# Optimization experiments

Hardware: AMD Instinct MI355X
Metric: run time of the kernel (lower is better)

The kernel has to match this reference:

```python
import jax, jax.numpy as jnp
import numpy as np

WS = 16      # window_size
FW = 1       # focal_window -> 3x3 grid of focal windows
FF = 2       # focal_factor (avg-pool for non-center windows)
NH = 8       # num_heads

_OFFSETS = [(di, dj) for di in range(-FW, FW + 1) for dj in range(-FW, FW + 1)]
# tokens contributed by each focal window (center keeps full res, neighbors pooled)
_COUNTS = np.array([WS * WS if (di == 0 and dj == 0) else (WS // FF) ** 2 for di, dj in _OFFSETS])
# center window gets zero bias, peripheral windows get -position_bias (intent of add_focal_bias)
_MULTS = np.array([0.0 if (di == 0 and dj == 0) else -1.0 for di, dj in _OFFSETS], dtype=np.float32)


def _gather_focal(x):
    """x: (B,H,W,C) -> (B*nW, kv_len, C) focal key/value tokens per window."""
    B, H, W, C = x.shape
    nH, nWg = H // WS, W // WS
    xp = jnp.pad(x, ((0, 0), (WS, WS), (WS, WS), (0, 0)), mode='reflect')
    # padded window grid: (B, nH+2, nWg+2, WS, WS, C)
    g = xp.reshape(B, nH + 2, WS, nWg + 2, WS, C).transpose(0, 1, 3, 2, 4, 5)
    parts = []
    for di, dj in _OFFSETS:
        w = g[:, 1 + di:1 + di + nH, 1 + dj:1 + dj + nWg]  # (B,nH,nWg,WS,WS,C)
        if di == 0 and dj == 0:
            t = w.reshape(B, nH, nWg, WS * WS, C)
        else:
            p = WS // FF  # avg_pool2d(kernel=stride=FF)
            t = w.reshape(B, nH, nWg, p, FF, p, FF, C).mean(axis=(4, 6)).reshape(B, nH, nWg, p * p, C)
        parts.append(t)
    kv = jnp.concatenate(parts, axis=3)  # (B,nH,nWg,kv_len,C)
    return kv.reshape(B * nH * nWg, -1, C)


def _bias_tokens(position_bias):
    # (NH, 9) -> (NH, kv_len): per-focal-window bias broadcast over its tokens
    scaled = position_bias * jnp.asarray(_MULTS)[None, :]
    return jnp.repeat(scaled, _COUNTS, axis=1)


def reference(x, Wq, bq, Wk, bk, Wv, bv, Wo, bo, position_bias):
    B, H, W, C = x.shape
    hd = C // NH
    scale = hd ** -0.5
    nH, nWg = H // WS, W // WS
    # window partition: (B*nW, WS*WS, C)
    xw = x.reshape(B, nH, WS, nWg, WS, C).transpose(0, 1, 3, 2, 4, 5).reshape(-1, WS * WS, C)
    kv = _gather_focal(x)  # (B*nW, kv_len, C)
    q = (xw @ Wq + bq).reshape(-1, WS * WS, NH, hd).transpose(0, 2, 1, 3)
    k = (kv @ Wk + bk).reshape(kv.shape[0], -1, NH, hd).transpose(0, 2, 1, 3)
    v = (kv @ Wv + bv).reshape(kv.shape[0], -1, NH, hd).transpose(0, 2, 1, 3)
    attn = jnp.einsum('whqd,whkd->whqk', q, k) * scale
    attn = attn + _bias_tokens(position_bias)[None, :, None, :]
    attn = jax.nn.softmax(attn, axis=-1)
    out = jnp.einsum('whqk,whkd->whqd', attn, v).transpose(0, 2, 1, 3).reshape(-1, WS * WS, C)
    out = out @ Wo + bo
    # window reverse
    out = out.reshape(B, nH, nWg, WS, WS, C).transpose(0, 1, 3, 2, 4, 5).reshape(B, H, W, C)
    return out


def setup_inputs() -> dict:
    key = jax.random.key(0)
    ks = jax.random.split(key, 10)
    D = 384
    w = lambda k: jax.random.normal(k, (D, D), dtype=jnp.float32) * 0.02
    b = lambda k: jax.random.normal(k, (D,), dtype=jnp.float32) * 0.02
    return {
        'x': jax.random.normal(ks[0], (2, 128, 128, D), dtype=jnp.float32),
        'Wq': w(ks[1]), 'bq': b(ks[2]),
        'Wk': w(ks[3]), 'bk': b(ks[4]),
        'Wv': w(ks[5]), 'bv': b(ks[6]),
        'Wo': w(ks[7]), 'bo': b(ks[8]),
        'position_bias': jax.random.normal(ks[9], (NH, 9), dtype=jnp.float32) * 0.02,
    }
```

## Files before the change

### kernel.cpp

```cpp
#include <hip/hip_runtime.h>
#include <hip/hip_bf16.h>

#define NTOK 32768
#define LOG2E 1.4426950408889634f

typedef __attribute__((ext_vector_type(8))) short bf16x8;
typedef __attribute__((ext_vector_type(4))) float f32x4;

__device__ __forceinline__ float bf2f(unsigned short u) {
  return __uint_as_float(((unsigned int)u) << 16);
}
__device__ __forceinline__ unsigned short f2bf(float f) {
  union { __hip_bfloat16 h; unsigned short u; } cv;
  cv.h = __float2bfloat16(f);
  return cv.u;
}
__device__ __forceinline__ unsigned cvt_pk_bf16(float lo, float hi) {
  unsigned r;
  asm("v_cvt_pk_bf16_f32 %0, %1, %2" : "=v"(r) : "v"(lo), "v"(hi));
  return r;
}
__device__ __forceinline__ float fast_exp2(float x) {
#if __has_builtin(__builtin_amdgcn_exp2f)
  return __builtin_amdgcn_exp2f(x);
#else
  return exp2f(x);
#endif
}

__device__ __forceinline__ void gload16(const void* g, void* l) {
  __builtin_amdgcn_global_load_lds(
      (const __attribute__((address_space(1))) unsigned int*)(unsigned long long)g,
      (__attribute__((address_space(3))) unsigned int*)(unsigned long long)l, 16, 0, 0);
}

__global__ __launch_bounds__(256) void convert_x(const float* __restrict__ x,
                                                 unsigned short* __restrict__ xb) {
  const int i = (blockIdx.x * 256 + threadIdx.x) * 8;
  float4 a = *(const float4*)(x + i);
  float4 b = *(const float4*)(x + i + 4);
  *(ushort4*)(xb + i)     = make_ushort4(f2bf(a.x), f2bf(a.y), f2bf(a.z), f2bf(a.w));
  *(ushort4*)(xb + i + 4) = make_ushort4(f2bf(b.x), f2bf(b.y), f2bf(b.z), f2bf(b.w));
}

__global__ __launch_bounds__(256) void transpose_w(const float* __restrict__ Wq,
                                                   const float* __restrict__ Wk,
                                                   const float* __restrict__ Wv,
                                                   const float* __restrict__ Wo,
                                                   unsigned short* __restrict__ Wt) {
  __shared__ float tile[32][33];
  const int wsel = blockIdx.z;
  const float* W = (wsel == 0) ? Wq : (wsel == 1) ? Wk : (wsel == 2) ? Wv : Wo;
  unsigned short* out = Wt + (size_t)wsel * 147456;
  const int k0 = blockIdx.x * 32, n0 = blockIdx.y * 32;
  const int r = threadIdx.x >> 3, c4 = (threadIdx.x & 7) * 4;
  float4 v = *(const float4*)&W[(size_t)(k0 + r) * 384 + n0 + c4];
  tile[r][c4 + 0] = v.x; tile[r][c4 + 1] = v.y; tile[r][c4 + 2] = v.z; tile[r][c4 + 3] = v.w;
  __syncthreads();
  ushort4 o = make_ushort4(f2bf(tile[c4 + 0][r]), f2bf(tile[c4 + 1][r]),
                           f2bf(tile[c4 + 2][r]), f2bf(tile[c4 + 3][r]));
  *(ushort4*)&out[(size_t)(n0 + r) * 384 + k0 + c4] = o;
}

__global__ __launch_bounds__(192) void pool_kernel(const unsigned short* __restrict__ xb,
                                                   unsigned short* __restrict__ P) {
  const int unit = blockIdx.x * 192 + threadIdx.x;
  const int cell = unit / 48;
  const int c8 = (unit - cell * 48) * 8;
  const int b = cell / 6400;
  const int rem = cell - b * 6400;
  const int p0 = rem / 80, p1 = rem - p0 * 80;
  const int i0 = 2 * p0 - 16, i1 = i0 + 1;
  const int j0 = 2 * p1 - 16, j1 = j0 + 1;
  const int r0 = i0 < 0 ? -i0 : (i0 > 127 ? 254 - i0 : i0);
  const int r1 = i1 < 0 ? -i1 : (i1 > 127 ? 254 - i1 : i1);
  const int c0 = j0 < 0 ? -j0 : (j0 > 127 ? 254 - j0 : j0);
  const int c1 = j1 < 0 ? -j1 : (j1 > 127 ? 254 - j1 : j1);
  uint4 u00 = *(const uint4*)(xb + ((size_t)((b * 128 + r0) * 128 + c0)) * 384 + c8);
  uint4 u01 = *(const uint4*)(xb + ((size_t)((b * 128 + r0) * 128 + c1)) * 384 + c8);
  uint4 u10 = *(const uint4*)(xb + ((size_t)((b * 128 + r1) * 128 + c0)) * 384 + c8);
  uint4 u11 = *(const uint4*)(xb + ((size_t)((b * 128 + r1) * 128 + c1)) * 384 + c8);
  const unsigned short* a0 = (const unsigned short*)&u00;
  const unsigned short* a1 = (const unsigned short*)&u01;
  const unsigned short* a2 = (const unsigned short*)&u10;
  const unsigned short* a3 = (const unsigned short*)&u11;
  unsigned short o[8];
  #pragma unroll
  for (int j = 0; j < 8; ++j)
    o[j] = f2bf(0.25f * (bf2f(a0[j]) + bf2f(a1[j]) + bf2f(a2[j]) + bf2f(a3[j])));
  uint4 ov;
  unsigned short* op = (unsigned short*)&ov;
  #pragma unroll
  for (int j = 0; j < 8; ++j) op[j] = o[j];
  *(uint4*)(P + (size_t)cell * 384 + c8) = ov;
}

__global__ __launch_bounds__(256) void mfma_proj_fused(
    const unsigned short* __restrict__ xb, const unsigned short* __restrict__ P,
    const unsigned short* __restrict__ Wt,
    const float* __restrict__ bq, const float* __restrict__ bk, const float* __restrict__ bv,
    unsigned short* __restrict__ Qb, unsigned short* __restrict__ Kcat,
    unsigned short* __restrict__ Vcat) {
  const int bid = blockIdx.x;
  const unsigned short* X;
  int wsel, colblk, yy; size_t off;
  if (bid < 2304) {
    const int xx = bid % 9; yy = bid / 9;
    X = xb; wsel = xx / 3; colblk = xx % 3; off = 0;
  } else {
    const int r = bid - 2304; const int xx = r % 6; yy = r / 6;
    X = P; wsel = 1 + xx / 3; colblk = xx % 3; off = (size_t)NTOK * 384;
  }
  const float* bias = (wsel == 0) ? bq : (wsel == 1) ? bk : bv;
  unsigned short* Y = ((wsel == 0) ? Qb : (wsel == 1) ? Kcat : Vcat) + off;
  const unsigned short* Wm = Wt + (size_t)wsel * 147456;
  const int n0 = colblk * 128;
  const int m0 = yy * 128;

  __shared__ __attribute__((aligned(16))) unsigned short As[2][128 * 32];
  __shared__ __attribute__((aligned(16))) unsigned short Bs[2][128 * 32];
  const int t = threadIdx.x;
  const int w = t >> 6, l = t & 63, l15 = l & 15, g = l >> 4;
  const int wm = w >> 1, wn = w & 1;
  const int srow = (w * 2) * 16 + (l >> 2), srow2 = (w * 2 + 1) * 16 + (l >> 2);
  const int skc = (l & 3) * 8;

  f32x4 acc[4][4];
  #pragma unroll
  for (int i = 0; i < 4; ++i)
    #pragma unroll
    for (int j = 0; j < 4; ++j) acc[i][j] = {0.f, 0.f, 0.f, 0.f};

  {
    gload16(X  + (size_t)(m0 + srow)  * 384 + skc, &As[0][(w * 2)     * 512]);
    gload16(X  + (size_t)(m0 + srow2) * 384 + skc, &As[0][(w * 2 + 1) * 512]);
    gload16(Wm + (size_t)(n0 + srow)  * 384 + skc, &Bs[0][(w * 2)     * 512]);
    gload16(Wm + (size_t)(n0 + srow2) * 384 + skc, &Bs[0][(w * 2 + 1) * 512]);
  }
  asm volatile("s_waitcnt vmcnt(0)" ::: "memory");
  __builtin_amdgcn_s_barrier();
  __builtin_amdgcn_sched_barrier(0);

  int cur = 0;
  for (int kt = 0; kt < 12; ++kt) {
    if (kt < 11) {
      const int k0 = (kt + 1) * 32;
      gload16(X  + (size_t)(m0 + srow)  * 384 + k0 + skc, &As[cur ^ 1][(w * 2)     * 512]);
      gload16(X  + (size_t)(m0 + srow2) * 384 + k0 + skc, &As[cur ^ 1][(w * 2 + 1) * 512]);
      gload16(Wm + (size_t)(n0 + srow)  * 384 + k0 + skc, &Bs[cur ^ 1][(w * 2)     * 512]);
      gload16(Wm + (size_t)(n0 + srow2) * 384 + k0 + skc, &Bs[cur ^ 1][(w * 2 + 1) * 512]);
    }
    bf16x8 af[4], bfr[4];
    #pragma unroll
    for (int mi = 0; mi < 4; ++mi)
      af[mi] = *(const bf16x8*)(&As[cur][(wm * 64 + mi * 16 + l15) * 32 + g * 8]);
    #pragma unroll
    for (int nj = 0; nj < 4; ++nj)
      bfr[nj] = *(const bf16x8*)(&Bs[cur][(wn * 64 + nj * 16 + l15) * 32 + g * 8]);
    #pragma unroll
    for (int mi = 0; mi < 4; ++mi)
      #pragma unroll
      for (int nj = 0; nj < 4; ++nj)
        acc[mi][nj] = __builtin_amdgcn_mfma_f32_16x16x32_bf16(af[mi], bfr[nj], acc[mi][nj], 0, 0, 0);
    if (kt < 11) {
      asm volatile("s_waitcnt vmcnt(0)" ::: "memory");
      __builtin_amdgcn_s_barrier();
      __builtin_amdgcn_sched_barrier(0);
      cur ^= 1;
    }
  }

  float bv4[4];
  #pragma unroll
  for (int nj = 0; nj < 4; ++nj) bv4[nj] = bias[n0 + wn * 64 + nj * 16 + l15];
  #pragma unroll
  for (int mi = 0; mi < 4; ++mi)
    #pragma unroll
    for (int nj = 0; nj < 4; ++nj)
      #pragma unroll
      for (int r = 0; r < 4; ++r) {
        const size_t row = m0 + wm * 64 + mi * 16 + g * 4 + r;
        const size_t col = n0 + wn * 64 + nj * 16 + l15;
        Y[row * 384 + col] = f2bf(acc[mi][nj][r] + bv4[nj]);
      }
}

__global__ __launch_bounds__(256) void mfma_proj_out(const unsigned short* __restrict__ X,
                                                     const unsigned short* __restrict__ Wm,
                                                     const float* __restrict__ bias,
                                                     float* __restrict__ Y) {
  const int n0 = blockIdx.x * 128, m0 = blockIdx.y * 128;
  __shared__ __attribute__((aligned(16))) unsigned short As[2][128 * 32];
  __shared__ __attribute__((aligned(16))) unsigned short Bs[2][128 * 32];
  const int t = threadIdx.x;
  const int w = t >> 6, l = t & 63, l15 = l & 15, g = l >> 4;
  const int wm = w >> 1, wn = w & 1;
  const int srow = (w * 2) * 16 + (l >> 2), srow2 = (w * 2 + 1) * 16 + (l >> 2);
  const int skc = (l & 3) * 8;

  f32x4 acc[4][4];
  #pragma unroll
  for (int i = 0; i < 4; ++i)
    #pragma unroll
    for (int j = 0; j < 4; ++j) acc[i][j] = {0.f, 0.f, 0.f, 0.f};

  {
    gload16(X  + (size_t)(m0 + srow)  * 384 + skc, &As[0][(w * 2)     * 512]);
    gload16(X  + (size_t)(m0 + srow2) * 384 + skc, &As[0][(w * 2 + 1) * 512]);
    gload16(Wm + (size_t)(n0 + srow)  * 384 + skc, &Bs[0][(w * 2)     * 512]);
    gload16(Wm + (size_t)(n0 + srow2) * 384 + skc, &Bs[0][(w * 2 + 1) * 512]);
  }
  asm volatile("s_waitcnt vmcnt(0)" ::: "memory");
  __builtin_amdgcn_s_barrier();
  __builtin_amdgcn_sched_barrier(0);

  int cur = 0;
  for (int kt = 0; kt < 12; ++kt) {
    if (kt < 11) {
      const int k0 = (kt + 1) * 32;
      gload16(X  + (size_t)(m0 + srow)  * 384 + k0 + skc, &As[cur ^ 1][(w * 2)     * 512]);
      gload16(X  + (size_t)(m0 + srow2) * 384 + k0 + skc, &As[cur ^ 1][(w * 2 + 1) * 512]);
      gload16(Wm + (size_t)(n0 + srow)  * 384 + k0 + skc, &Bs[cur ^ 1][(w * 2)     * 512]);
      gload16(Wm + (size_t)(n0 + srow2) * 384 + k0 + skc, &Bs[cur ^ 1][(w * 2 + 1) * 512]);
    }
    bf16x8 af[4], bfr[4];
    #pragma unroll
    for (int mi = 0; mi < 4; ++mi)
      af[mi] = *(const bf16x8*)(&As[cur][(wm * 64 + mi * 16 + l15) * 32 + g * 8]);
    #pragma unroll
    for (int nj = 0; nj < 4; ++nj)
      bfr[nj] = *(const bf16x8*)(&Bs[cur][(wn * 64 + nj * 16 + l15) * 32 + g * 8]);
    #pragma unroll
    for (int mi = 0; mi < 4; ++mi)
      #pragma unroll
      for (int nj = 0; nj < 4; ++nj)
        acc[mi][nj] = __builtin_amdgcn_mfma_f32_16x16x32_bf16(af[mi], bfr[nj], acc[mi][nj], 0, 0, 0);
    if (kt < 11) {
      asm volatile("s_waitcnt vmcnt(0)" ::: "memory");
      __builtin_amdgcn_s_barrier();
      __builtin_amdgcn_sched_barrier(0);
      cur ^= 1;
    }
  }

  float bv4[4];
  #pragma unroll
  for (int nj = 0; nj < 4; ++nj) bv4[nj] = bias[n0 + wn * 64 + nj * 16 + l15];
  #pragma unroll
  for (int mi = 0; mi < 4; ++mi)
    #pragma unroll
    for (int nj = 0; nj < 4; ++nj)
      #pragma unroll
      for (int r = 0; r < 4; ++r) {
        const size_t row = m0 + wm * 64 + mi * 16 + g * 4 + r;
        const size_t col = n0 + wn * 64 + nj * 16 + l15;
        Y[row * 384 + col] = acc[mi][nj][r] + bv4[nj];
      }
}

__global__ __launch_bounds__(256) void attn_mfma(const unsigned short* __restrict__ Qg,
                                                 const unsigned short* __restrict__ Kc,
                                                 const unsigned short* __restrict__ Vc,
                                                 const float* __restrict__ pb,
                                                 unsigned short* __restrict__ AttO) {
  __shared__ unsigned short kvb[768];
  __shared__ float tb2s[12];
  __shared__ __attribute__((aligned(16))) unsigned short Ks[2][3072];
  __shared__ __attribute__((aligned(16))) unsigned short Vt[2][64 * 68];

  const int t = threadIdx.x;
  const int head = blockIdx.x >> 7, win = blockIdx.x & 127;
  const int b = win >> 6, wrem = win & 63, wi = wrem >> 3, wj = wrem & 7;
  const int w = t >> 6, l = t & 63, l15 = l & 15, g = l >> 4;
  const int hb = head * 48;

  for (int j = t; j < 768; j += 256) {
    int o, within;
    if (j < 256)      { o = j >> 6;               within = j & 63; }
    else if (j < 512) { o = 4;                    within = j - 256; }
    else              { o = 5 + ((j - 512) >> 6); within = j & 63; }
    int tok;
    if (o == 4) {
      int r = within >> 4, c = within & 15;
      tok = (b * 128 + wi * 16 + r) * 128 + wj * 16 + c;
    } else {
      int di = o / 3 - 1, dj = o - (o / 3) * 3 - 1;
      int t0 = within >> 3, t1 = within & 7;
      int p0 = 8 * (1 + di + wi) + t0, p1 = 8 * (1 + dj + wj) + t1;
      tok = NTOK + (b * 80 + p0) * 80 + p1;
    }
    kvb[j] = (unsigned short)tok;
  }
  if (t < 12) {
    int o = (t < 4) ? t : ((t < 8) ? 4 : t - 3);
    tb2s[t] = (o == 4) ? 0.0f : (-pb[head * 9 + o] * LOG2E);
  }
  for (int idx = t; idx < 2 * 16 * 68; idx += 256) {
    const int bu = idx / 1088, rem = idx - bu * 1088;
    const int rr = rem / 68, cc = rem - rr * 68;
    Vt[bu][(48 + rr) * 68 + cc] = (rr == 0) ? 0x3F80 : 0;
  }

  const float SCALE2 = 0.14433756729740643f * LOG2E;
  const bf16x8 z8 = {0, 0, 0, 0, 0, 0, 0, 0};

  bf16x8 qf[4][2];
  #pragma unroll
  for (int nf = 0; nf < 4; ++nf) {
    const int tok = ((b * 128 + wi * 16 + w * 4 + nf) * 128 + wj * 16 + l15);
    const unsigned short* qp = Qg + (size_t)tok * 384 + hb;
    qf[nf][0] = *(const bf16x8*)(qp + g * 8);
    qf[nf][1] = (g < 2) ? *(const bf16x8*)(qp + 32 + g * 8) : z8;
  }

  f32x4 Oacc[4][4];
  #pragma unroll
  for (int mo = 0; mo < 4; ++mo)
    #pragma unroll
    for (int nf = 0; nf < 4; ++nf) Oacc[mo][nf] = {0.f, 0.f, 0.f, 0.f};

  __syncthreads();

  uint4 va0, va1;
  {
    const int kvb0 = (int)kvb[l] * 384 + hb;
    gload16(Kc + kvb0 + w * 8, &Ks[0][w * 512]);
    if (w < 2) gload16(Kc + kvb0 + (4 + w) * 8, &Ks[0][(4 + w) * 512]);
    va0 = *(const uint4*)(Vc + kvb0 + w * 8);
    va1 = (w < 2) ? *(const uint4*)(Vc + kvb0 + (4 + w) * 8) : make_uint4(0, 0, 0, 0);
  }

  for (int T = 0; T < 12; ++T) {
    const int buf = T & 1;
    asm volatile("s_waitcnt vmcnt(0)" ::: "memory");
    {
      const unsigned short* u0 = (const unsigned short*)&va0;
      #pragma unroll
      for (int s = 0; s < 8; ++s) Vt[buf][(w * 8 + s) * 68 + l] = u0[s];
      if (w < 2) {
        const unsigned short* u1 = (const unsigned short*)&va1;
        #pragma unroll
        for (int s = 0; s < 8; ++s) Vt[buf][((4 + w) * 8 + s) * 68 + l] = u1[s];
      }
    }
    __syncthreads();
    if (T < 11) {
      const int kvb2 = (int)kvb[(T + 1) * 64 + l] * 384 + hb;
      gload16(Kc + kvb2 + w * 8, &Ks[buf ^ 1][w * 512]);
      if (w < 2) gload16(Kc + kvb2 + (4 + w) * 8, &Ks[buf ^ 1][(4 + w) * 512]);
      va0 = *(const uint4*)(Vc + kvb2 + w * 8);
      if (w < 2) va1 = *(const uint4*)(Vc + kvb2 + (4 + w) * 8);
    }

    const float tb = tb2s[T];
    #pragma unroll
    for (int h = 0; h < 2; ++h) {
      bf16x8 ka[2][2];
      #pragma unroll
      for (int mi = 0; mi < 2; ++mi) {
        const int krow = h * 32 + mi * 16 + l15;
        ka[mi][0] = *(const bf16x8*)&Ks[buf][g * 512 + krow * 8];
        ka[mi][1] = *(const bf16x8*)&Ks[buf][(4 + (g & 1)) * 512 + krow * 8];
      }
      f32x4 sf[2][4];
      #pragma unroll
      for (int mi = 0; mi < 2; ++mi)
        #pragma unroll
        for (int nf = 0; nf < 4; ++nf) sf[mi][nf] = {0.f, 0.f, 0.f, 0.f};
      __builtin_amdgcn_s_setprio(1);
      #pragma unroll
      for (int mi = 0; mi < 2; ++mi)
        #pragma unroll
        for (int nf = 0; nf < 4; ++nf) {
          sf[mi][nf] = __builtin_amdgcn_mfma_f32_16x16x32_bf16(ka[mi][0], qf[nf][0], sf[mi][nf], 0, 0, 0);
          sf[mi][nf] = __builtin_amdgcn_mfma_f32_16x16x32_bf16(ka[mi][1], qf[nf][1], sf[mi][nf], 0, 0, 0);
        }
      __builtin_amdgcn_s_setprio(0);

      bf16x8 pbf[4];
      #pragma unroll
      for (int nf = 0; nf < 4; ++nf) {
        float p[8];
        #pragma unroll
        for (int r = 0; r < 4; ++r) {
          p[r]     = fast_exp2(fmaf(sf[0][nf][r], SCALE2, tb));
          p[4 + r] = fast_exp2(fmaf(sf[1][nf][r], SCALE2, tb));
        }
        unsigned a0 = cvt_pk_bf16(p[0], p[1]);
        unsigned a1 = cvt_pk_bf16(p[2], p[3]);
        unsigned b0 = cvt_pk_bf16(p[4], p[5]);
        unsigned b1 = cvt_pk_bf16(p[6], p[7]);
        asm("v_permlane32_swap_b32 %0, %1" : "+v"(a0), "+v"(b0));
        asm("v_permlane32_swap_b32 %0, %1" : "+v"(a1), "+v"(b1));
        asm("v_permlane16_swap_b32 %0, %1" : "+v"(a0), "+v"(b0));
        asm("v_permlane16_swap_b32 %0, %1" : "+v"(a1), "+v"(b1));
        union { bf16x8 v; unsigned u[4]; } cv;
        cv.u[0] = a0; cv.u[1] = a1; cv.u[2] = b0; cv.u[3] = b1;
        pbf[nf] = cv.v;
      }

      #pragma unroll
      for (int mo = 0; mo < 4; ++mo) {
        const unsigned short* vp = &Vt[buf][(mo * 16 + l15) * 68 + h * 32 + g * 8];
        union { bf16x8 v; ushort4 u[2]; } cv;
        cv.u[0] = *(const ushort4*)vp;
        cv.u[1] = *(const ushort4*)(vp + 4);
        bf16x8 va = cv.v;
        __builtin_amdgcn_s_setprio(1);
        #pragma unroll
        for (int nf = 0; nf < 4; ++nf)
          Oacc[mo][nf] = __builtin_amdgcn_mfma_f32_16x16x32_bf16(va, pbf[nf], Oacc[mo][nf], 0, 0, 0);
        __builtin_amdgcn_s_setprio(0);
      }
    }
  }

  #pragma unroll
  for (int nf = 0; nf < 4; ++nf) {
    const float denom = __shfl(Oacc[3][nf][0], l15, 64);
    const float inv = 1.0f / denom;
    const int tok = ((b * 128 + wi * 16 + w * 4 + nf) * 128 + wj * 16 + l15);
    unsigned short* op = AttO + (size_t)tok * 384 + hb;
    #pragma unroll
    for (int mo = 0; mo < 3; ++mo) {
      uint2 u;
      u.x = cvt_pk_bf16(Oacc[mo][nf][0] * inv, Oacc[mo][nf][1] * inv);
      u.y = cvt_pk_bf16(Oacc[mo][nf][2] * inv, Oacc[mo][nf][3] * inv);
      *(uint2*)(op + mo * 16 + g * 4) = u;
    }
  }
}

extern "C" void kernel_launch(void* const* d_in, const int* in_sizes, int n_in,
                              void* d_out, int out_size, void* d_ws, size_t ws_size,
                              hipStream_t stream) {
  const float* x  = (const float*)d_in[0];
  const float* Wq = (const float*)d_in[1];
  const float* bq = (const float*)d_in[2];
  const float* Wk = (const float*)d_in[3];
  const float* bk = (const float*)d_in[4];
  const float* Wv = (const float*)d_in[5];
  const float* bv = (const float*)d_in[6];
  const float* Wo = (const float*)d_in[7];
  const float* bo = (const float*)d_in[8];
  const float* pb = (const float*)d_in[9];

  char* ws = (char*)d_ws;
  unsigned short* Wt   = (unsigned short*)(ws);
  unsigned short* P    = (unsigned short*)(ws + 1179648ull);
  unsigned short* Kcat = (unsigned short*)(ws + 11010048ull);
  unsigned short* Vcat = (unsigned short*)(ws + 46006272ull);
  unsigned short* xb   = (unsigned short*)(ws + 81002496ull);
  unsigned short* AttO = xb;
  unsigned short* Qb   = (unsigned short*)d_out;

  convert_x<<<6144, 256, 0, stream>>>(x, xb);
  pool_kernel<<<3200, 192, 0, stream>>>(xb, P);
  transpose_w<<<dim3(12, 12, 4), 256, 0, stream>>>(Wq, Wk, Wv, Wo, Wt);
  mfma_proj_fused<<<2904, 256, 0, stream>>>(xb, P, Wt, bq, bk, bv, Qb, Kcat, Vcat);
  attn_mfma<<<1024, 256, 0, stream>>>(Qb, Kcat, Vcat, pb, AttO);
  mfma_proj_out<<<dim3(3, 256), 256, 0, stream>>>(AttO, Wt + 3 * 147456, bo, (float*)d_out);
}
```

Baseline: 189.1 us.

## Triple-buffer GEMM K-tiles with two-deep prefetch and remap attention block order

Both projection GEMM kernels move from double to triple buffering in shared memory. Two K-tiles are prefetched ahead, and each iteration waits with vmcnt(4) rather than vmcnt(0), so one tile's loads stay in flight while the current tile is computed. The attention kernel also remaps block index to (head, window) so that 8 consecutive blocks share a head and cover neighbouring windows, aiming for better L2 reuse of overlapping K/V. The extra buffer raises LDS use per block, which may lower occupancy.

```diff
diff --git a/kernel.cpp b/kernel.cpp
--- a/kernel.cpp
+++ b/kernel.cpp
@@ -117,8 +117,8 @@
   const int n0 = colblk * 128;
   const int m0 = yy * 128;
 
-  __shared__ __attribute__((aligned(16))) unsigned short As[2][128 * 32];
-  __shared__ __attribute__((aligned(16))) unsigned short Bs[2][128 * 32];
+  __shared__ __attribute__((aligned(16))) unsigned short As[3][128 * 32];
+  __shared__ __attribute__((aligned(16))) unsigned short Bs[3][128 * 32];
   const int t = threadIdx.x;
   const int w = t >> 6, l = t & 63, l15 = l & 15, g = l >> 4;
   const int wm = w >> 1, wn = w & 1;
@@ -131,25 +131,29 @@
     #pragma unroll
     for (int j = 0; j < 4; ++j) acc[i][j] = {0.f, 0.f, 0.f, 0.f};
 
-  {
-    gload16(X  + (size_t)(m0 + srow)  * 384 + skc, &As[0][(w * 2)     * 512]);
-    gload16(X  + (size_t)(m0 + srow2) * 384 + skc, &As[0][(w * 2 + 1) * 512]);
-    gload16(Wm + (size_t)(n0 + srow)  * 384 + skc, &Bs[0][(w * 2)     * 512]);
-    gload16(Wm + (size_t)(n0 + srow2) * 384 + skc, &Bs[0][(w * 2 + 1) * 512]);
-  }
-  asm volatile("s_waitcnt vmcnt(0)" ::: "memory");
-  __builtin_amdgcn_s_barrier();
-  __builtin_amdgcn_sched_barrier(0);
-
-  int cur = 0;
+  #pragma unroll
+  for (int pt = 0; pt < 2; ++pt) {
+    const int k0 = pt * 32;
+    gload16(X  + (size_t)(m0 + srow)  * 384 + k0 + skc, &As[pt][(w * 2)     * 512]);
+    gload16(X  + (size_t)(m0 + srow2) * 384 + k0 + skc, &As[pt][(w * 2 + 1) * 512]);
+    gload16(Wm + (size_t)(n0 + srow)  * 384 + k0 + skc, &Bs[pt][(w * 2)     * 512]);
+    gload16(Wm + (size_t)(n0 + srow2) * 384 + k0 + skc, &Bs[pt][(w * 2 + 1) * 512]);
+  }
+
   for (int kt = 0; kt < 12; ++kt) {
-    if (kt < 11) {
-      const int k0 = (kt + 1) * 32;
-      gload16(X  + (size_t)(m0 + srow)  * 384 + k0 + skc, &As[cur ^ 1][(w * 2)     * 512]);
-      gload16(X  + (size_t)(m0 + srow2) * 384 + k0 + skc, &As[cur ^ 1][(w * 2 + 1) * 512]);
-      gload16(Wm + (size_t)(n0 + srow)  * 384 + k0 + skc, &Bs[cur ^ 1][(w * 2)     * 512]);
-      gload16(Wm + (size_t)(n0 + srow2) * 384 + k0 + skc, &Bs[cur ^ 1][(w * 2 + 1) * 512]);
-    }
+    if (kt < 11) asm volatile("s_waitcnt vmcnt(4)" ::: "memory");
+    else         asm volatile("s_waitcnt vmcnt(0)" ::: "memory");
+    __builtin_amdgcn_s_barrier();
+    __builtin_amdgcn_sched_barrier(0);
+    if (kt < 10) {
+      const int k0 = (kt + 2) * 32;
+      const int bnext = (kt + 2) % 3;
+      gload16(X  + (size_t)(m0 + srow)  * 384 + k0 + skc, &As[bnext][(w * 2)     * 512]);
+      gload16(X  + (size_t)(m0 + srow2) * 384 + k0 + skc, &As[bnext][(w * 2 + 1) * 512]);
+      gload16(Wm + (size_t)(n0 + srow)  * 384 + k0 + skc, &Bs[bnext][(w * 2)     * 512]);
+      gload16(Wm + (size_t)(n0 + srow2) * 384 + k0 + skc, &Bs[bnext][(w * 2 + 1) * 512]);
+    }
+    const int cur = kt % 3;
     bf16x8 af[4], bfr[4];
     #pragma unroll
     for (int mi = 0; mi < 4; ++mi)
@@ -162,12 +166,6 @@
       #pragma unroll
       for (int nj = 0; nj < 4; ++nj)
         acc[mi][nj] = __builtin_amdgcn_mfma_f32_16x16x32_bf16(af[mi], bfr[nj], acc[mi][nj], 0, 0, 0);
-    if (kt < 11) {
-      asm volatile("s_waitcnt vmcnt(0)" ::: "memory");
-      __builtin_amdgcn_s_barrier();
-      __builtin_amdgcn_sched_barrier(0);
-      cur ^= 1;
-    }
   }
 
   float bv4[4];
@@ -190,8 +188,8 @@
                                                      const float* __restrict__ bias,
                                                      float* __restrict__ Y) {
   const int n0 = blockIdx.x * 128, m0 = blockIdx.y * 128;
-  __shared__ __attribute__((aligned(16))) unsigned short As[2][128 * 32];
-  __shared__ __attribute__((aligned(16))) unsigned short Bs[2][128 * 32];
+  __shared__ __attribute__((aligned(16))) unsigned short As[3][128 * 32];
+  __shared__ __attribute__((aligned(16))) unsigned short Bs[3][128 * 32];
   const int t = threadIdx.x;
   const int w = t >> 6, l = t & 63, l15 = l & 15, g = l >> 4;
   const int wm = w >> 1, wn = w & 1;
@@ -204,25 +202,29 @@
     #pragma unroll
     for (int j = 0; j < 4; ++j) acc[i][j] = {0.f, 0.f, 0.f, 0.f};
 
-  {
-    gload16(X  + (size_t)(m0 + srow)  * 384 + skc, &As[0][(w * 2)     * 512]);
-    gload16(X  + (size_t)(m0 + srow2) * 384 + skc, &As[0][(w * 2 + 1) * 512]);
-    gload16(Wm + (size_t)(n0 + srow)  * 384 + skc, &Bs[0][(w * 2)     * 512]);
-    gload16(Wm + (size_t)(n0 + srow2) * 384 + skc, &Bs[0][(w * 2 + 1) * 512]);
-  }
-  asm volatile("s_waitcnt vmcnt(0)" ::: "memory");
-  __builtin_amdgcn_s_barrier();
-  __builtin_amdgcn_sched_barrier(0);
-
-  int cur = 0;
+  #pragma unroll
+  for (int pt = 0; pt < 2; ++pt) {
+    const int k0 = pt * 32;
+    gload16(X  + (size_t)(m0 + srow)  * 384 + k0 + skc, &As[pt][(w * 2)     * 512]);
+    gload16(X  + (size_t)(m0 + srow2) * 384 + k0 + skc, &As[pt][(w * 2 + 1) * 512]);
+    gload16(Wm + (size_t)(n0 + srow)  * 384 + k0 + skc, &Bs[pt][(w * 2)     * 512]);
+    gload16(Wm + (size_t)(n0 + srow2) * 384 + k0 + skc, &Bs[pt][(w * 2 + 1) * 512]);
+  }
+
   for (int kt = 0; kt < 12; ++kt) {
-    if (kt < 11) {
-      const int k0 = (kt + 1) * 32;
-      gload16(X  + (size_t)(m0 + srow)  * 384 + k0 + skc, &As[cur ^ 1][(w * 2)     * 512]);
-      gload16(X  + (size_t)(m0 + srow2) * 384 + k0 + skc, &As[cur ^ 1][(w * 2 + 1) * 512]);
-      gload16(Wm + (size_t)(n0 + srow)  * 384 + k0 + skc, &Bs[cur ^ 1][(w * 2)     * 512]);
-      gload16(Wm + (size_t)(n0 + srow2) * 384 + k0 + skc, &Bs[cur ^ 1][(w * 2 + 1) * 512]);
-    }
+    if (kt < 11) asm volatile("s_waitcnt vmcnt(4)" ::: "memory");
+    else         asm volatile("s_waitcnt vmcnt(0)" ::: "memory");
+    __builtin_amdgcn_s_barrier();
+    __builtin_amdgcn_sched_barrier(0);
+    if (kt < 10) {
+      const int k0 = (kt + 2) * 32;
+      const int bnext = (kt + 2) % 3;
+      gload16(X  + (size_t)(m0 + srow)  * 384 + k0 + skc, &As[bnext][(w * 2)     * 512]);
+      gload16(X  + (size_t)(m0 + srow2) * 384 + k0 + skc, &As[bnext][(w * 2 + 1) * 512]);
+      gload16(Wm + (size_t)(n0 + srow)  * 384 + k0 + skc, &Bs[bnext][(w * 2)     * 512]);
+      gload16(Wm + (size_t)(n0 + srow2) * 384 + k0 + skc, &Bs[bnext][(w * 2 + 1) * 512]);
+    }
+    const int cur = kt % 3;
     bf16x8 af[4], bfr[4];
     #pragma unroll
     for (int mi = 0; mi < 4; ++mi)
@@ -235,12 +237,6 @@
       #pragma unroll
       for (int nj = 0; nj < 4; ++nj)
         acc[mi][nj] = __builtin_amdgcn_mfma_f32_16x16x32_bf16(af[mi], bfr[nj], acc[mi][nj], 0, 0, 0);
-    if (kt < 11) {
-      asm volatile("s_waitcnt vmcnt(0)" ::: "memory");
-      __builtin_amdgcn_s_barrier();
-      __builtin_amdgcn_sched_barrier(0);
-      cur ^= 1;
-    }
   }
 
   float bv4[4];
@@ -269,7 +265,9 @@
   __shared__ __attribute__((aligned(16))) unsigned short Vt[2][64 * 68];
 
   const int t = threadIdx.x;
-  const int head = blockIdx.x >> 7, win = blockIdx.x & 127;
+  const int bid = blockIdx.x;
+  const int head = (bid >> 3) & 7;
+  const int win  = (bid & 7) + 8 * (bid >> 6);
   const int b = win >> 6, wrem = win & 63, wi = wrem >> 3, wj = wrem & 7;
   const int w = t >> 6, l = t & 63, l15 = l & 15, g = l >> 4;
   const int hb = head * 48;
```

Result: no change. 186.7 us (-1.3%).
